# Optimization experiments

Hardware: AMD Instinct MI355X
Metric: run time of the kernel (lower is better)

## Reference

```python
import jax, jax.numpy as jnp
import numpy as np

N = 50000   # nodes
E = 800000  # edges


def gcn_conv(x, src, dst, W, b):
    # PyG GCNConv: h = x @ W; add self-loops; symmetric norm D^-1/2 A D^-1/2; + bias
    h = x @ W                                              # [N, dout]
    deg = jax.ops.segment_sum(jnp.ones((E,), h.dtype), dst, num_segments=N) + 1.0  # +1 self-loop
    inv_sqrt = jax.lax.rsqrt(deg)                          # [N]
    coef = inv_sqrt[src] * inv_sqrt[dst]                   # [E]
    agg = jax.ops.segment_sum(h[src] * coef[:, None], dst, num_segments=N)
    agg = agg + h * (inv_sqrt * inv_sqrt)[:, None]         # self-loop contribution
    return agg + b


def setup_inputs() -> dict:
    key = jax.random.key(0)
    ks = jax.random.split(key, 6)
    x = jax.random.normal(ks[0], (N, 128), jnp.float32)
    edge_index = jax.random.randint(ks[1], (2, E), 0, N, jnp.int32)
    W1 = jax.random.normal(ks[2], (128, 128), jnp.float32) * (1.0 / np.sqrt(128.0))
    b1 = jnp.zeros((128,), jnp.float32)
    W2 = jax.random.normal(ks[3], (128, 64), jnp.float32) * (1.0 / np.sqrt(128.0))
    b2 = jnp.zeros((64,), jnp.float32)
    return {"x": x, "edge_index": edge_index, "W1": W1, "b1": b1, "W2": W2, "b2": b2}


def reference(x, edge_index, W1, b1, W2, b2):
    src, dst = edge_index[0], edge_index[1]
    h = jax.nn.relu(gcn_conv(x, src, dst, W1, b1))
    # dropout is identity in eval mode (training=False)
    return gcn_conv(h, src, dst, W2, b2)
```

## Files before the change

kernel.cpp:

```cpp
#include <hip/hip_runtime.h>

typedef unsigned int uint32;
typedef unsigned short ush;
typedef __attribute__((ext_vector_type(8))) short short8;
typedef __attribute__((ext_vector_type(4))) float f32x4;

__device__ __forceinline__ ush f2bf(float f) {
    union { float f; uint32 u; } v; v.f = f;
    uint32 r = v.u + 0x7fffu + ((v.u >> 16) & 1u);
    return (ush)(r >> 16);
}
__device__ __forceinline__ float bfl(uint32 u) {
    union { uint32 u; float f; } v; v.u = u << 16; return v.f;
}
__device__ __forceinline__ float bfh(uint32 u) {
    union { uint32 u; float f; } v; v.u = u & 0xffff0000u; return v.f;
}

#define BSH 6
#define NBMAX 1024
#define CHUNK 4096


__global__ void k_zerob(int* __restrict__ b, int nb) {
    int i = blockIdx.x * 256 + threadIdx.x;
    if (i < nb) b[i] = 0;
}

__global__ __launch_bounds__(256) void k_bcount(const int* __restrict__ dst,
                                                int* __restrict__ bcnt, int e, int nb) {
    __shared__ int cnt[NBMAX];
    for (int i = threadIdx.x; i < nb; i += 256) cnt[i] = 0;
    __syncthreads();
    int base = blockIdx.x * CHUNK;
    int end = min(e, base + CHUNK);
    for (int i = base + threadIdx.x; i < end; i += 256)
        atomicAdd(&cnt[dst[i] >> BSH], 1);
    __syncthreads();
    for (int i = threadIdx.x; i < nb; i += 256) {
        int c = cnt[i];
        if (c) atomicAdd(&bcnt[i], c);
    }
}

__global__ void k_bscan(const int* __restrict__ bcnt, int* __restrict__ bstart,
                        int* __restrict__ bcur, int nb, int e) {
    __shared__ int s[256];
    __shared__ int carry;
    int tid = threadIdx.x;
    if (tid == 0) carry = 0;
    __syncthreads();
    for (int base = 0; base < nb; base += 256) {
        int v = (base + tid < nb) ? bcnt[base + tid] : 0;
        s[tid] = v;
        __syncthreads();
        for (int off = 1; off < 256; off <<= 1) {
            int t = (tid >= off) ? s[tid - off] : 0;
            __syncthreads();
            s[tid] += t;
            __syncthreads();
        }
        int ex = s[tid] - v + carry;
        if (base + tid < nb) { bstart[base + tid] = ex; bcur[base + tid] = ex; }
        __syncthreads();
        if (tid == 0) carry += s[255];
        __syncthreads();
    }
    if (tid == 0) bstart[nb] = e;
}

__global__ __launch_bounds__(256) void k_binA2(const int* __restrict__ src,
                                               const int* __restrict__ dst,
                                               int* __restrict__ bcur,
                                               int2* __restrict__ rec, int e, int nb) {
    __shared__ int cnt[NBMAX];
    __shared__ int bas[NBMAX];
    __shared__ int off[NBMAX];
    for (int i = threadIdx.x; i < nb; i += 256) { cnt[i] = 0; off[i] = 0; }
    __syncthreads();
    int base = blockIdx.x * CHUNK;
    int end = min(e, base + CHUNK);
    for (int i = base + threadIdx.x; i < end; i += 256)
        atomicAdd(&cnt[dst[i] >> BSH], 1);
    __syncthreads();
    for (int i = threadIdx.x; i < nb; i += 256) {
        int c = cnt[i];
        if (c) bas[i] = atomicAdd(&bcur[i], c);
    }
    __syncthreads();
    for (int i = base + threadIdx.x; i < end; i += 256) {
        int s = src[i];
        int d = dst[i];
        int b = d >> BSH;
        int p = bas[b] + atomicAdd(&off[b], 1);
        rec[p] = make_int2(s, d);
    }
}

__global__ __launch_bounds__(256) void k_degB(const int2* __restrict__ rec,
                                              const int* __restrict__ bstart,
                                              int* __restrict__ rowstart,
                                              float* __restrict__ inv, int n, int e) {
    __shared__ int cnt[64];
    int b = blockIdx.x;
    int st = bstart[b], en = bstart[b + 1];
    if (threadIdx.x < 64) cnt[threadIdx.x] = 0;
    __syncthreads();
    for (int i = st + threadIdx.x; i < en; i += 256)
        atomicAdd(&cnt[rec[i].y & 63], 1);
    __syncthreads();
    if (threadIdx.x < 64) {
        int c = cnt[threadIdx.x];
        int incl = c;
        #pragma unroll
        for (int o2 = 1; o2 < 64; o2 <<= 1) {
            int t = __shfl_up(incl, o2, 64);
            if ((int)threadIdx.x >= o2) incl += t;
        }
        int node = (b << BSH) + threadIdx.x;
        if (node < n) {
            rowstart[node] = st + incl - c;
            inv[node] = rsqrtf((float)c + 1.0f);
        }
    }
    if (b == 0 && threadIdx.x == 0) rowstart[n] = e;
}

__global__ __launch_bounds__(256) void k_fillB2(const int2* __restrict__ rec,
                                                const int* __restrict__ bstart,
                                                const int* __restrict__ rowstart,
                                                const float* __restrict__ inv,
                                                int2* __restrict__ es, int n) {
    __shared__ int cur[64];
    int b = blockIdx.x;
    int st = bstart[b], en = bstart[b + 1];
    if (threadIdx.x < 64) {
        int node = (b << BSH) + threadIdx.x;
        cur[threadIdx.x] = (node < n) ? (rowstart[node] - st) : 0;
    }
    __syncthreads();
    for (int i = st + threadIdx.x; i < en; i += 256) {
        int2 r = rec[i];
        int slot = atomicAdd(&cur[r.y & 63], 1);
        es[st + slot] = make_int2(r.x, __float_as_int(inv[r.x]));
    }
}

__global__ void k_wcvt(const float* __restrict__ W, ush* __restrict__ wh,
                       ush* __restrict__ wl, int csh, int total) {
    int i = blockIdx.x * 256 + threadIdx.x;
    if (i >= total) return;
    int k = i >> csh;
    int col = i & ((1 << csh) - 1);
    float w = W[i];
    ush hi = f2bf(w);
    ush lo = f2bf(w - bfl((uint32)hi));
    int byte = ((col * 128 + k) * 2) ^ ((col & 7) << 4);
    *(ush*)((char*)wh + byte) = hi;
    *(ush*)((char*)wl + byte) = lo;
}

template <int COUT>
__global__ __launch_bounds__(256) void k_gemm_mfma(const float* __restrict__ x,
                                                   const ush* __restrict__ gwh,
                                                   const ush* __restrict__ gwl,
                                                   ush* __restrict__ h, int n) {
    constexpr int CT = COUT / 32;
    __shared__ short xh[128 * 128];
    __shared__ short xl[128 * 128];
    __shared__ short wh[COUT * 128];
    __shared__ short wl[COUT * 128];
    int tid = threadIdx.x;
    int row0 = blockIdx.x * 128;

    for (int i = tid; i < COUT * 16; i += 256) {
        ((short8*)wh)[i] = ((const short8*)gwh)[i];
        ((short8*)wl)[i] = ((const short8*)gwl)[i];
    }
    #pragma unroll
    for (int i = 0; i < 8; ++i) {
        int rl = (tid >> 4) + i * 16;
        int k0 = (tid & 15) * 8;
        int row = row0 + rl;
        float f[8];
        if (row < n) {
            float4 p0 = *(const float4*)&x[(size_t)row * 128 + k0];
            float4 p1 = *(const float4*)&x[(size_t)row * 128 + k0 + 4];
            f[0] = p0.x; f[1] = p0.y; f[2] = p0.z; f[3] = p0.w;
            f[4] = p1.x; f[5] = p1.y; f[6] = p1.z; f[7] = p1.w;
        } else {
            #pragma unroll
            for (int j = 0; j < 8; ++j) f[j] = 0.f;
        }
        short8 hi, lo;
        #pragma unroll
        for (int j = 0; j < 8; ++j) {
            ush hb = f2bf(f[j]);
            hi[j] = (short)hb;
            lo[j] = (short)f2bf(f[j] - bfl((uint32)hb));
        }
        int byte = (rl * 256 + k0 * 2) ^ ((rl & 7) << 4);
        *(short8*)((char*)xh + byte) = hi;
        *(short8*)((char*)xl + byte) = lo;
    }
    __syncthreads();

    int wid = tid >> 6, lane = tid & 63;
    int wr = wid >> 1, wc = wid & 1;
    int arow = wr * 64;
    int bcol = wc * (COUT / 2);
    int l15 = lane & 15, kg = lane >> 4;

    f32x4 acc[4][CT];
    #pragma unroll
    for (int rt = 0; rt < 4; ++rt)
        #pragma unroll
        for (int ct = 0; ct < CT; ++ct)
            acc[rt][ct] = (f32x4){0.f, 0.f, 0.f, 0.f};

    #pragma unroll
    for (int ks = 0; ks < 4; ++ks) {
        short8 ah[4], al[4];
        #pragma unroll
        for (int rt = 0; rt < 4; ++rt) {
            int r = arow + rt * 16 + l15;
            int byte = (r * 256 + ks * 64 + kg * 16) ^ ((r & 7) << 4);
            ah[rt] = *(const short8*)((const char*)xh + byte);
            al[rt] = *(const short8*)((const char*)xl + byte);
        }
        #pragma unroll
        for (int ct = 0; ct < CT; ++ct) {
            int c = bcol + ct * 16 + l15;
            int byte = (c * 256 + ks * 64 + kg * 16) ^ ((c & 7) << 4);
            short8 bh = *(const short8*)((const char*)wh + byte);
            short8 bl = *(const short8*)((const char*)wl + byte);
            #pragma unroll
            for (int rt = 0; rt < 4; ++rt) {
                acc[rt][ct] = __builtin_amdgcn_mfma_f32_16x16x32_bf16(ah[rt], bh, acc[rt][ct], 0, 0, 0);
                acc[rt][ct] = __builtin_amdgcn_mfma_f32_16x16x32_bf16(al[rt], bh, acc[rt][ct], 0, 0, 0);
                acc[rt][ct] = __builtin_amdgcn_mfma_f32_16x16x32_bf16(ah[rt], bl, acc[rt][ct], 0, 0, 0);
            }
        }
    }

    int rq = kg * 4;
    #pragma unroll
    for (int rt = 0; rt < 4; ++rt) {
        #pragma unroll
        for (int ct = 0; ct < CT; ++ct) {
            int col = bcol + ct * 16 + l15;
            #pragma unroll
            for (int q = 0; q < 4; ++q) {
                int row = row0 + arow + rt * 16 + rq + q;
                if (row < n) h[(size_t)row * COUT + col] = f2bf(acc[rt][ct][q]);
            }
        }
    }
}

template <int COLS, bool RELU>
__global__ __launch_bounds__(256) void k_gather(const ush* __restrict__ h,
                                                const int* __restrict__ rowstart,
                                                const int2* __restrict__ es,
                                                const float* __restrict__ inv,
                                                const float* __restrict__ bias,
                                                float* __restrict__ out, int n) {
    int wave = threadIdx.x >> 6;
    int lane = threadIdx.x & 63;
    int node = blockIdx.x * 4 + wave;
    if (node >= n) return;
    int s0 = rowstart[node];
    int s1 = rowstart[node + 1];
    float iv = inv[node];

    if constexpr (COLS == 128) {
        int c = lane * 2;
        float accx = 0.f, accy = 0.f;
        int i = s0;
        for (; i + 8 <= s1; i += 8) {
            int    a[8];
            float  w[8];
            uint32 u[8];
            #pragma unroll
            for (int j = 0; j < 8; ++j) {
                int2 r = es[i + j];
                a[j] = r.x;
                w[j] = __int_as_float(r.y);
            }
            #pragma unroll
            for (int j = 0; j < 8; ++j)
                u[j] = *(const uint32*)&h[(size_t)a[j] * 128 + c];
            #pragma unroll
            for (int j = 0; j < 8; ++j) {
                accx += w[j] * bfl(u[j]);
                accy += w[j] * bfh(u[j]);
            }
        }
        for (; i < s1; ++i) {
            int2 r = es[i];
            uint32 u = *(const uint32*)&h[(size_t)r.x * 128 + c];
            float w = __int_as_float(r.y);
            accx += w * bfl(u);
            accy += w * bfh(u);
        }
        uint32 us = *(const uint32*)&h[(size_t)node * 128 + c];
        float2 bb = *(const float2*)&bias[c];
        float ox = iv * accx + iv * iv * bfl(us) + bb.x;
        float oy = iv * accy + iv * iv * bfh(us) + bb.y;
        if (RELU) { ox = fmaxf(ox, 0.f); oy = fmaxf(oy, 0.f); }
        *(float2*)&out[node * 128 + c] = make_float2(ox, oy);
    } else {
        int c = lane;
        float acc = 0.f;
        int i = s0;
        for (; i + 8 <= s1; i += 8) {
            int   a[8];
            float w[8];
            ush   u[8];
            #pragma unroll
            for (int j = 0; j < 8; ++j) {
                int2 r = es[i + j];
                a[j] = r.x;
                w[j] = __int_as_float(r.y);
            }
            #pragma unroll
            for (int j = 0; j < 8; ++j)
                u[j] = h[(size_t)a[j] * 64 + c];
            #pragma unroll
            for (int j = 0; j < 8; ++j)
                acc += w[j] * bfl((uint32)u[j]);
        }
        for (; i < s1; ++i) {
            int2 r = es[i];
            acc += __int_as_float(r.y) * bfl((uint32)h[(size_t)r.x * 64 + c]);
        }
        float self = bfl((uint32)h[(size_t)node * 64 + c]);
        float o = iv * acc + iv * iv * self + bias[c];
        if (RELU) o = fmaxf(o, 0.f);
        out[node * 64 + c] = o;
    }
}


extern "C" void kernel_launch(void* const* d_in, const int* in_sizes, int n_in,
                              void* d_out, int out_size, void* d_ws, size_t ws_size,
                              hipStream_t stream) {
    const float* x  = (const float*)d_in[0];
    const int*   ei = (const int*)d_in[1];
    const float* W1 = (const float*)d_in[2];
    const float* b1 = (const float*)d_in[3];
    const float* W2 = (const float*)d_in[4];
    const float* b2 = (const float*)d_in[5];
    float* out = (float*)d_out;

    const int N = in_sizes[0] / 128;
    const int E = in_sizes[1] / 2;
    const int NB = (N + 63) >> BSH;
    const int* src = ei;
    const int* dstp = ei + E;

    char* p = (char*)d_ws;
    auto take = [&](size_t bytes) {
        char* r = p;
        p += (bytes + 255) & ~(size_t)255;
        return r;
    };
    float* inv      = (float*)take((size_t)N * 4);
    int*   rowstart = (int*)take((size_t)(N + 1) * 4);
    int*   bcnt     = (int*)take((size_t)NB * 4);
    int*   bstart   = (int*)take((size_t)(NB + 1) * 4);
    int*   bcur     = (int*)take((size_t)NB * 4);
    int2*  rec      = (int2*)take((size_t)E * 8);
    int2*  es       = (int2*)take((size_t)E * 8);
    ush*   w1h      = (ush*)take(16384 * 2);
    ush*   w1l      = (ush*)take(16384 * 2);
    ush*   w2h      = (ush*)take(8192 * 2);
    ush*   w2l      = (ush*)take(8192 * 2);
    ush*   h1       = (ush*)take((size_t)N * 128 * 2);
    float* act1     = (float*)take((size_t)N * 128 * 4);
    ush*   h2       = h1;

    const int nbC = (E + CHUNK - 1) / CHUNK;

    k_zerob <<<(NB + 255) / 256, 256, 0, stream>>>(bcnt, NB);
    k_bcount<<<nbC, 256, 0, stream>>>(dstp, bcnt, E, NB);
    k_bscan <<<1, 256, 0, stream>>>(bcnt, bstart, bcur, NB, E);
    k_binA2 <<<nbC, 256, 0, stream>>>(src, dstp, bcur, rec, E, NB);
    k_degB  <<<NB, 256, 0, stream>>>(rec, bstart, rowstart, inv, N, E);
    k_fillB2<<<NB, 256, 0, stream>>>(rec, bstart, rowstart, inv, es, N);

    k_wcvt<<<64, 256, 0, stream>>>(W1, w1h, w1l, 7, 16384);
    k_wcvt<<<32, 256, 0, stream>>>(W2, w2h, w2l, 6, 8192);

    const int gb = (N + 127) / 128;
    k_gemm_mfma<128><<<gb, 256, 0, stream>>>(x, w1h, w1l, h1, N);
    k_gather<128, true><<<(N + 3) / 4, 256, 0, stream>>>(h1, rowstart, es, inv, b1, act1, N);
    k_gemm_mfma<64><<<gb, 256, 0, stream>>>(act1, w2h, w2l, h2, N);
    k_gather<64, false><<<(N + 3) / 4, 256, 0, stream>>>(h2, rowstart, es, inv, b2, out, N);
}
```

Before: 240.1 us.

## Pack bin records, fuse weight conversion into GEMMs, store layer-1 activations as bf16

Bin records are packed into one 32-bit word (16-bit source id plus 6-bit local dst), which halves traffic for the bucketing pass. The separate weight-conversion kernels are removed and each GEMM block converts W itself. The first gather now writes bf16 activations, and the second GEMM reads them directly using only the high part of the split, which halves activation traffic but lowers precision. CHUNK is also halved. Packing the source id into 16 bits truncates it for N=50000, since ids above 65535 would be lost, and node ids up to 49999 only just fit.

```diff
diff --git a/kernel.cpp b/kernel.cpp
--- a/kernel.cpp
+++ b/kernel.cpp
@@ -19,7 +19,7 @@
 
 #define BSH 6
 #define NBMAX 1024
-#define CHUNK 4096
+#define CHUNK 2048
 
 
 __global__ void k_zerob(int* __restrict__ b, int nb) {
@@ -72,7 +72,7 @@
 __global__ __launch_bounds__(256) void k_binA2(const int* __restrict__ src,
                                                const int* __restrict__ dst,
                                                int* __restrict__ bcur,
-                                               int2* __restrict__ rec, int e, int nb) {
+                                               int* __restrict__ rec, int e, int nb) {
     __shared__ int cnt[NBMAX];
     __shared__ int bas[NBMAX];
     __shared__ int off[NBMAX];
@@ -93,11 +93,11 @@
         int d = dst[i];
         int b = d >> BSH;
         int p = bas[b] + atomicAdd(&off[b], 1);
-        rec[p] = make_int2(s, d);
-    }
-}
-
-__global__ __launch_bounds__(256) void k_degB(const int2* __restrict__ rec,
+        rec[p] = (s & 0xFFFF) | ((d & 63) << 16);
+    }
+}
+
+__global__ __launch_bounds__(256) void k_degB(const int* __restrict__ rec,
                                               const int* __restrict__ bstart,
                                               int* __restrict__ rowstart,
                                               float* __restrict__ inv, int n, int e) {
@@ -107,7 +107,7 @@
     if (threadIdx.x < 64) cnt[threadIdx.x] = 0;
     __syncthreads();
     for (int i = st + threadIdx.x; i < en; i += 256)
-        atomicAdd(&cnt[rec[i].y & 63], 1);
+        atomicAdd(&cnt[(rec[i] >> 16) & 63], 1);
     __syncthreads();
     if (threadIdx.x < 64) {
         int c = cnt[threadIdx.x];
@@ -126,7 +126,7 @@
     if (b == 0 && threadIdx.x == 0) rowstart[n] = e;
 }
 
-__global__ __launch_bounds__(256) void k_fillB2(const int2* __restrict__ rec,
+__global__ __launch_bounds__(256) void k_fillB2(const int* __restrict__ rec,
                                                 const int* __restrict__ bstart,
                                                 const int* __restrict__ rowstart,
                                                 const float* __restrict__ inv,
@@ -140,32 +140,17 @@
     }
     __syncthreads();
     for (int i = st + threadIdx.x; i < en; i += 256) {
-        int2 r = rec[i];
-        int slot = atomicAdd(&cur[r.y & 63], 1);
-        es[st + slot] = make_int2(r.x, __float_as_int(inv[r.x]));
-    }
-}
-
-__global__ void k_wcvt(const float* __restrict__ W, ush* __restrict__ wh,
-                       ush* __restrict__ wl, int csh, int total) {
-    int i = blockIdx.x * 256 + threadIdx.x;
-    if (i >= total) return;
-    int k = i >> csh;
-    int col = i & ((1 << csh) - 1);
-    float w = W[i];
-    ush hi = f2bf(w);
-    ush lo = f2bf(w - bfl((uint32)hi));
-    int byte = ((col * 128 + k) * 2) ^ ((col & 7) << 4);
-    *(ush*)((char*)wh + byte) = hi;
-    *(ush*)((char*)wl + byte) = lo;
-}
-
-template <int COUT>
-__global__ __launch_bounds__(256) void k_gemm_mfma(const float* __restrict__ x,
-                                                   const ush* __restrict__ gwh,
-                                                   const ush* __restrict__ gwl,
-                                                   ush* __restrict__ h, int n) {
-    constexpr int CT = COUT / 32;
+        int r = rec[i];
+        int s = r & 0xFFFF;
+        int slot = atomicAdd(&cur[(r >> 16) & 63], 1);
+        es[st + slot] = make_int2(s, __float_as_int(inv[s]));
+    }
+}
+
+__global__ __launch_bounds__(256) void k_gemm1m(const float* __restrict__ x,
+                                                const float* __restrict__ W,
+                                                ush* __restrict__ h, int n) {
+    constexpr int COUT = 128, CT = 4;
     __shared__ short xh[128 * 128];
     __shared__ short xl[128 * 128];
     __shared__ short wh[COUT * 128];
@@ -173,9 +158,13 @@
     int tid = threadIdx.x;
     int row0 = blockIdx.x * 128;
 
-    for (int i = tid; i < COUT * 16; i += 256) {
-        ((short8*)wh)[i] = ((const short8*)gwh)[i];
-        ((short8*)wl)[i] = ((const short8*)gwl)[i];
+    for (int i = tid; i < 128 * COUT; i += 256) {
+        int k = i >> 7, col = i & 127;
+        float w = W[i];
+        ush hb = f2bf(w);
+        int byte = ((col * 128 + k) * 2) ^ ((col & 7) << 4);
+        *(ush*)((char*)wh + byte) = hb;
+        *(ush*)((char*)wl + byte) = f2bf(w - bfl((uint32)hb));
     }
     #pragma unroll
     for (int i = 0; i < 8; ++i) {
@@ -206,9 +195,8 @@
     __syncthreads();
 
     int wid = tid >> 6, lane = tid & 63;
-    int wr = wid >> 1, wc = wid & 1;
-    int arow = wr * 64;
-    int bcol = wc * (COUT / 2);
+    int arow = (wid >> 1) * 64;
+    int bcol = (wid & 1) * (COUT / 2);
     int l15 = lane & 15, kg = lane >> 4;
 
     f32x4 acc[4][CT];
@@ -245,7 +233,7 @@
 
     int rq = kg * 4;
     #pragma unroll
-    for (int rt = 0; rt < 4; ++rt) {
+    for (int rt = 0; rt < 4; ++rt)
         #pragma unroll
         for (int ct = 0; ct < CT; ++ct) {
             int col = bcol + ct * 16 + l15;
@@ -255,16 +243,96 @@
                 if (row < n) h[(size_t)row * COUT + col] = f2bf(acc[rt][ct][q]);
             }
         }
-    }
-}
-
-template <int COLS, bool RELU>
+}
+
+__global__ __launch_bounds__(256) void k_gemm2m(const ush* __restrict__ a,
+                                                const float* __restrict__ W,
+                                                ush* __restrict__ h, int n) {
+    constexpr int COUT = 64, CT = 2;
+    __shared__ short xh[128 * 128];
+    __shared__ short wh[COUT * 128];
+    __shared__ short wl[COUT * 128];
+    int tid = threadIdx.x;
+    int row0 = blockIdx.x * 128;
+
+    for (int i = tid; i < 128 * COUT; i += 256) {
+        int k = i >> 6, col = i & 63;
+        float w = W[i];
+        ush hb = f2bf(w);
+        int byte = ((col * 128 + k) * 2) ^ ((col & 7) << 4);
+        *(ush*)((char*)wh + byte) = hb;
+        *(ush*)((char*)wl + byte) = f2bf(w - bfl((uint32)hb));
+    }
+    #pragma unroll
+    for (int i = 0; i < 8; ++i) {
+        int rl = (tid >> 4) + i * 16;
+        int k0 = (tid & 15) * 8;
+        int row = row0 + rl;
+        short8 v;
+        #pragma unroll
+        for (int j = 0; j < 8; ++j) v[j] = 0;
+        if (row < n) v = *(const short8*)&a[(size_t)row * 128 + k0];
+        int byte = (rl * 256 + k0 * 2) ^ ((rl & 7) << 4);
+        *(short8*)((char*)xh + byte) = v;
+    }
+    __syncthreads();
+
+    int wid = tid >> 6, lane = tid & 63;
+    int arow = (wid >> 1) * 64;
+    int bcol = (wid & 1) * (COUT / 2);
+    int l15 = lane & 15, kg = lane >> 4;
+
+    f32x4 acc[4][CT];
+    #pragma unroll
+    for (int rt = 0; rt < 4; ++rt)
+        #pragma unroll
+        for (int ct = 0; ct < CT; ++ct)
+            acc[rt][ct] = (f32x4){0.f, 0.f, 0.f, 0.f};
+
+    #pragma unroll
+    for (int ks = 0; ks < 4; ++ks) {
+        short8 ah[4];
+        #pragma unroll
+        for (int rt = 0; rt < 4; ++rt) {
+            int r = arow + rt * 16 + l15;
+            int byte = (r * 256 + ks * 64 + kg * 16) ^ ((r & 7) << 4);
+            ah[rt] = *(const short8*)((const char*)xh + byte);
+        }
+        #pragma unroll
+        for (int ct = 0; ct < CT; ++ct) {
+            int c = bcol + ct * 16 + l15;
+            int byte = (c * 256 + ks * 64 + kg * 16) ^ ((c & 7) << 4);
+            short8 bh = *(const short8*)((const char*)wh + byte);
+            short8 bl = *(const short8*)((const char*)wl + byte);
+            #pragma unroll
+            for (int rt = 0; rt < 4; ++rt) {
+                acc[rt][ct] = __builtin_amdgcn_mfma_f32_16x16x32_bf16(ah[rt], bh, acc[rt][ct], 0, 0, 0);
+                acc[rt][ct] = __builtin_amdgcn_mfma_f32_16x16x32_bf16(ah[rt], bl, acc[rt][ct], 0, 0, 0);
+            }
+        }
+    }
+
+    int rq = kg * 4;
+    #pragma unroll
+    for (int rt = 0; rt < 4; ++rt)
+        #pragma unroll
+        for (int ct = 0; ct < CT; ++ct) {
+            int col = bcol + ct * 16 + l15;
+            #pragma unroll
+            for (int q = 0; q < 4; ++q) {
+                int row = row0 + arow + rt * 16 + rq + q;
+                if (row < n) h[(size_t)row * COUT + col] = f2bf(acc[rt][ct][q]);
+            }
+        }
+}
+
+template <int COLS, bool RELU, bool OUTBF>
 __global__ __launch_bounds__(256) void k_gather(const ush* __restrict__ h,
                                                 const int* __restrict__ rowstart,
                                                 const int2* __restrict__ es,
                                                 const float* __restrict__ inv,
                                                 const float* __restrict__ bias,
-                                                float* __restrict__ out, int n) {
+                                                void* __restrict__ outp, int n) {
     int wave = threadIdx.x >> 6;
     int lane = threadIdx.x & 63;
     int node = blockIdx.x * 4 + wave;
@@ -308,7 +376,12 @@
         float ox = iv * accx + iv * iv * bfl(us) + bb.x;
         float oy = iv * accy + iv * iv * bfh(us) + bb.y;
         if (RELU) { ox = fmaxf(ox, 0.f); oy = fmaxf(oy, 0.f); }
-        *(float2*)&out[node * 128 + c] = make_float2(ox, oy);
+        if constexpr (OUTBF) {
+            uint32 pk = (uint32)f2bf(ox) | ((uint32)f2bf(oy) << 16);
+            *(uint32*)&((ush*)outp)[(size_t)node * 128 + c] = pk;
+        } else {
+            *(float2*)&((float*)outp)[(size_t)node * 128 + c] = make_float2(ox, oy);
+        }
     } else {
         int c = lane;
         float acc = 0.f;
@@ -337,7 +410,7 @@
         float self = bfl((uint32)h[(size_t)node * 64 + c]);
         float o = iv * acc + iv * iv * self + bias[c];
         if (RELU) o = fmaxf(o, 0.f);
-        out[node * 64 + c] = o;
+        ((float*)outp)[(size_t)node * 64 + c] = o;
     }
 }
 
@@ -370,14 +443,10 @@
     int*   bcnt     = (int*)take((size_t)NB * 4);
     int*   bstart   = (int*)take((size_t)(NB + 1) * 4);
     int*   bcur     = (int*)take((size_t)NB * 4);
-    int2*  rec      = (int2*)take((size_t)E * 8);
+    int*   rec      = (int*)take((size_t)E * 4);
     int2*  es       = (int2*)take((size_t)E * 8);
-    ush*   w1h      = (ush*)take(16384 * 2);
-    ush*   w1l      = (ush*)take(16384 * 2);
-    ush*   w2h      = (ush*)take(8192 * 2);
-    ush*   w2l      = (ush*)take(8192 * 2);
     ush*   h1       = (ush*)take((size_t)N * 128 * 2);
-    float* act1     = (float*)take((size_t)N * 128 * 4);
+    ush*   act1     = (ush*)take((size_t)N * 128 * 2);
     ush*   h2       = h1;
 
     const int nbC = (E + CHUNK - 1) / CHUNK;
@@ -389,12 +458,9 @@
     k_degB  <<<NB, 256, 0, stream>>>(rec, bstart, rowstart, inv, N, E);
     k_fillB2<<<NB, 256, 0, stream>>>(rec, bstart, rowstart, inv, es, N);
 
-    k_wcvt<<<64, 256, 0, stream>>>(W1, w1h, w1l, 7, 16384);
-    k_wcvt<<<32, 256, 0, stream>>>(W2, w2h, w2l, 6, 8192);
-
     const int gb = (N + 127) / 128;
-    k_gemm_mfma<128><<<gb, 256, 0, stream>>>(x, w1h, w1l, h1, N);
-    k_gather<128, true><<<(N + 3) / 4, 256, 0, stream>>>(h1, rowstart, es, inv, b1, act1, N);
-    k_gemm_mfma<64><<<gb, 256, 0, stream>>>(act1, w2h, w2l, h2, N);
-    k_gather<64, false><<<(N + 3) / 4, 256, 0, stream>>>(h2, rowstart, es, inv, b2, out, N);
-}
+    k_gemm1m<<<gb, 256, 0, stream>>>(x, W1, h1, N);
+    k_gather<128, true, true><<<(N + 3) / 4, 256, 0, stream>>>(h1, rowstart, es, inv, b1, act1, N);
+    k_gemm2m<<<gb, 256, 0, stream>>>(act1, W2, h2, N);
+    k_gather<64, false, false><<<(N + 3) / 4, 256, 0, stream>>>(h2, rowstart, es, inv, b2, out, N);
+}
```

Result: slower. 246.6 us (+2.7%).
